# Optimization experiments

Hardware: AMD Instinct MI355X
Metric: run time of the kernel (lower is better)

Reference implementation:

```python
import jax, jax.numpy as jnp
import numpy as np

INPUT_DIM = 384
H1, H2, BOTTLENECK = 512, 216, 10
NUM_ANNOTATORS = 2316
BATCH = 16384


def setup_inputs() -> dict:
    key = jax.random.key(0)
    ks = jax.random.split(key, 9)

    def lin(k, fan_in, fan_out):
        # torch nn.Linear default init: U(-1/sqrt(fan_in), 1/sqrt(fan_in))
        bound = 1.0 / np.sqrt(fan_in)
        kw, kb = jax.random.split(k)
        W = jax.random.uniform(kw, (fan_in, fan_out), jnp.float32, -bound, bound)
        b = jax.random.uniform(kb, (fan_out,), jnp.float32, -bound, bound)
        return W, b

    x = jax.random.normal(ks[0], (BATCH, INPUT_DIM), jnp.float32)
    W1, b1 = lin(ks[1], INPUT_DIM, H1)
    W2, b2 = lin(ks[2], H1, H2)
    W3, b3 = lin(ks[3], H2, BOTTLENECK)
    # 2316 heads of Linear(10, 1) stacked into a single (10, 2316) matrix + (2316,) bias
    Wh, bh = lin(ks[4], BOTTLENECK, NUM_ANNOTATORS)
    return {"x": x, "W1": W1, "b1": b1, "W2": W2, "b2": b2,
            "W3": W3, "b3": b3, "Wh": Wh, "bh": bh}


def reference(x, W1, b1, W2, b2, W3, b3, Wh, bh):
    # shared encoder (dropout is identity in eval mode)
    h = jax.nn.relu(x @ W1 + b1)            # [B, 512]
    h = jax.nn.relu(h @ W2 + b2)            # [B, 216]
    f = jax.nn.relu(h @ W3 + b3)            # [B, 10]
    # 2316 per-annotator heads fused into one GEMM: [B,10] @ [10,2316] + [2316]
    return f @ Wh + bh                      # [B, 2316]
```

## Files before the change

kernel.cpp:

```cpp
#include <hip/hip_runtime.h>
#include <hip/hip_bf16.h>
#include <stdint.h>

using f32x4  = __attribute__((ext_vector_type(4))) float;
using bf16x8 = __attribute__((ext_vector_type(8))) __bf16;
using u16x4  = __attribute__((ext_vector_type(4))) unsigned short;
using u16x8  = __attribute__((ext_vector_type(8))) unsigned short;

#define DEVFN static __device__ __forceinline__

constexpr int IND = 384, N1 = 512, N2R = 216, N2 = 256, NB = 10, NA = 2316;
constexpr int BATCH = 16384;
constexpr int RB  = 64;
constexpr int NC1 = 12;
constexpr int NC2 = 16;
constexpr int K3  = 224;

constexpr int WS_W1  = 0;
constexpr int WS_W2  = WS_W1 + NC1 * N1 * 32;
constexpr int WS_W3  = WS_W2 + NC2 * N2 * 32;
constexpr size_t WS_F_BYTE = 708864;
constexpr size_t WS_NEED   = WS_F_BYTE + (size_t)BATCH * 12 * 4;

constexpr int XT_OFF = 0;      constexpr int XT_ST = 784;
constexpr int W1T    = 51200;
constexpr int H1_OFF = 0;      constexpr int H1_ST = 1040;
constexpr int W2T    = 66560;
constexpr int H2_OFF = 0;      constexpr int H2_ST = 528;
constexpr int W3_OFF = 115712;
constexpr int F_OFF  = 122880; constexpr int F_ST  = 48;
constexpr int B1L    = 149504;
constexpr int B2L    = 151552;
constexpr int B3L    = 152576;
constexpr int LDS_E  = 152640;

DEVFN unsigned short bf16u(float f) {
    __hip_bfloat16 h = __float2bfloat16(f);
    unsigned short u; __builtin_memcpy(&u, &h, 2); return u;
}

DEVFN void mfma16(f32x4& d, bf16x8 a, bf16x8 b) {
    d = __builtin_amdgcn_mfma_f32_16x16x32_bf16(a, b, d, 0, 0, 0);
}

DEVFN void gll16(const void* g, void* lds) {
    __builtin_amdgcn_global_load_lds((const __attribute__((address_space(1))) void*)g,
                                     (__attribute__((address_space(3))) void*)lds, 16, 0, 0);
}

DEVFN void wait_vm4()   { asm volatile("s_waitcnt vmcnt(4)" ::: "memory"); }
DEVFN void wait_vm2()   { asm volatile("s_waitcnt vmcnt(2)" ::: "memory"); }
DEVFN void wait_vm0()   { asm volatile("s_waitcnt vmcnt(0)" ::: "memory"); }
DEVFN void wait_lgkm0() { asm volatile("s_waitcnt lgkmcnt(0)" ::: "memory"); }

__global__ __launch_bounds__(256)
void cvt_weights(const float* __restrict__ W1, const float* __restrict__ W2,
                 const float* __restrict__ W3,
                 unsigned short* __restrict__ ws)
{
    const int bid = blockIdx.x, tid = threadIdx.x;
    if (bid < 48) {
        const int c = bid >> 2, o = bid & 3;
        #pragma unroll
        for (int half = 0; half < 2; ++half) {
            const int col = half * 256 + tid;
            u16x8 v;
            #pragma unroll
            for (int s7 = 0; s7 < 8; ++s7)
                v[s7] = bf16u(W1[(size_t)(c * 32 + o * 8 + s7) * N1 + col]);
            *(u16x8*)(ws + WS_W1 + c * 16384 + col * 32 + ((o ^ (col & 3)) << 3)) = v;
        }
    } else if (bid < 112) {
        const int t = bid - 48;
        const int c = t >> 2, o = t & 3;
        const int col = tid;
        u16x8 v;
        #pragma unroll
        for (int s7 = 0; s7 < 8; ++s7) {
            int k = c * 32 + o * 8 + s7;
            v[s7] = (col < N2R) ? bf16u(W2[(size_t)k * N2R + col]) : (unsigned short)0;
        }
        *(u16x8*)(ws + WS_W2 + c * 8192 + col * 32 + ((o ^ (col & 3)) << 3)) = v;
    } else {
        for (int i = tid; i < 16 * K3; i += 256) {
            int col = i / K3, s = i - col * K3;
            int sb = s >> 5, r = s & 31;
            int k = sb * 32 + (((r >> 3) ^ (col & 3)) << 3) + (r & 7);
            float v = (col < NB && k < 216) ? W3[k * NB + col] : 0.f;
            ws[WS_W3 + i] = bf16u(v);
        }
    }
}

__global__ __launch_bounds__(512)
void encoder(const float* __restrict__ x,
             const float* __restrict__ b1g, const float* __restrict__ b2g,
             const float* __restrict__ b3g,
             const unsigned short* __restrict__ ws,
             float* __restrict__ fout)
{
    __shared__ __attribute__((aligned(16))) unsigned char smem[LDS_E];
    const int tid  = threadIdx.x;
    const int wave = tid >> 6;
    const int lane = tid & 63;
    const int l16  = lane & 15;
    const int lk   = lane >> 4;
    const int wr   = wave >> 2;
    const int wc   = wave & 3;
    const int row0 = blockIdx.x * RB;

    {
        const float4* xg = (const float4*)(x + (size_t)row0 * IND);
        #pragma unroll
        for (int i = 0; i < 12; ++i) {
            int j = tid + i * 512;
            float4 v = xg[j];
            int el = j * 4, r = el / IND, c = el - r * IND;
            u16x4 h;
            h[0] = bf16u(v.x); h[1] = bf16u(v.y); h[2] = bf16u(v.z); h[3] = bf16u(v.w);
            *(u16x4*)(smem + XT_OFF + r * XT_ST + c * 2) = h;
        }
        *(float*)(smem + B1L + tid * 4) = b1g[tid];
        if (tid < 256) *(float*)(smem + B2L + tid * 4) = (tid < N2R) ? b2g[tid] : 0.f;
        if (tid < 16)  *(float*)(smem + B3L + tid * 4) = (tid < NB)  ? b3g[tid] : 0.f;
    }
    __syncthreads();

    const unsigned char* wsW1 = (const unsigned char*)(ws + WS_W1);
    f32x4 acc1[2][8] = {};

    #pragma unroll
    for (int cc = 0; cc < 2; ++cc)
        #pragma unroll
        for (int o = 0; o < 4; ++o) {
            int wb = o * 8192 + wave * 1024;
            gll16(wsW1 + cc * 32768 + wb + lane * 16, smem + W1T + cc * 32768 + wb);
        }
    for (int c = 0; c < NC1; ++c) {
        if (c + 1 < NC1) wait_vm4(); else wait_vm0();
        __builtin_amdgcn_s_barrier();
        if (c + 2 < NC1) {
            const unsigned char* src = wsW1 + (size_t)(c + 2) * 32768;
            const int nxt = W1T + ((c + 2) % 3) * 32768;
            #pragma unroll
            for (int o = 0; o < 4; ++o) {
                int wb = o * 8192 + wave * 1024;
                gll16(src + wb + lane * 16, smem + nxt + wb);
            }
        }
        const int cur = W1T + (c % 3) * 32768;
        const int k0 = c * 32;
        bf16x8 a0 = *(const bf16x8*)(smem + XT_OFF + (wr * 32 + l16)      * XT_ST + (k0 + lk * 8) * 2);
        bf16x8 a1 = *(const bf16x8*)(smem + XT_OFF + (wr * 32 + 16 + l16) * XT_ST + (k0 + lk * 8) * 2);
        #pragma unroll
        for (int n = 0; n < 8; ++n) {
            int col = wc * 128 + n * 16 + l16;
            bf16x8 b = *(const bf16x8*)(smem + cur + col * 64 + ((lk ^ (col & 3)) << 4));
            mfma16(acc1[0][n], a0, b);
            mfma16(acc1[1][n], a1, b);
        }
    }
    __builtin_amdgcn_s_barrier();
    #pragma unroll
    for (int m = 0; m < 2; ++m)
        #pragma unroll
        for (int n = 0; n < 8; ++n) {
            int col = wc * 128 + n * 16 + l16;
            float bias = *(const float*)(smem + B1L + col * 4);
            #pragma unroll
            for (int e = 0; e < 4; ++e) {
                float v = fmaxf(acc1[m][n][e] + bias, 0.f);
                *(unsigned short*)(smem + H1_OFF + (wr * 32 + m * 16 + lk * 4 + e) * H1_ST + col * 2) = bf16u(v);
            }
        }
    wait_lgkm0();
    __builtin_amdgcn_s_barrier();

    const unsigned char* wsW2 = (const unsigned char*)(ws + WS_W2);
    f32x4 acc2[2][4] = {};

    #pragma unroll
    for (int cc = 0; cc < 2; ++cc)
        #pragma unroll
        for (int o = 0; o < 2; ++o) {
            int wb = o * 8192 + wave * 1024;
            gll16(wsW2 + cc * 16384 + wb + lane * 16, smem + W2T + cc * 16384 + wb);
        }
    for (int c = 0; c < NC2; ++c) {
        if (c + 1 < NC2) wait_vm2(); else wait_vm0();
        __builtin_amdgcn_s_barrier();
        if (c + 2 < NC2) {
            const unsigned char* src = wsW2 + (size_t)(c + 2) * 16384;
            const int nxt = W2T + ((c + 2) % 3) * 16384;
            #pragma unroll
            for (int o = 0; o < 2; ++o) {
                int wb = o * 8192 + wave * 1024;
                gll16(src + wb + lane * 16, smem + nxt + wb);
            }
        }
        const int cur = W2T + (c % 3) * 16384;
        const int k0 = c * 32;
        bf16x8 a0 = *(const bf16x8*)(smem + H1_OFF + (wr * 32 + l16)      * H1_ST + (k0 + lk * 8) * 2);
        bf16x8 a1 = *(const bf16x8*)(smem + H1_OFF + (wr * 32 + 16 + l16) * H1_ST + (k0 + lk * 8) * 2);
        #pragma unroll
        for (int n = 0; n < 4; ++n) {
            int col = wc * 64 + n * 16 + l16;
            bf16x8 b = *(const bf16x8*)(smem + cur + col * 64 + ((lk ^ (col & 3)) << 4));
            mfma16(acc2[0][n], a0, b);
            mfma16(acc2[1][n], a1, b);
        }
    }
    __builtin_amdgcn_s_barrier();
    #pragma unroll
    for (int m = 0; m < 2; ++m)
        #pragma unroll
        for (int n = 0; n < 4; ++n) {
            int col = wc * 64 + n * 16 + l16;
            float bias = *(const float*)(smem + B2L + col * 4);
            #pragma unroll
            for (int e = 0; e < 4; ++e) {
                float v = fmaxf(acc2[m][n][e] + bias, 0.f);
                *(unsigned short*)(smem + H2_OFF + (wr * 32 + m * 16 + lk * 4 + e) * H2_ST + col * 2) = bf16u(v);
            }
        }
    if (wave < 7)
        gll16((const unsigned char*)(ws + WS_W3) + wave * 1024 + lane * 16, smem + W3_OFF + wave * 1024);
    __syncthreads();

    f32x4 acc3[2] = {};
    #pragma unroll
    for (int c = 0; c < 7; ++c) {
        const int k0 = c * 32;
        bf16x8 a0 = *(const bf16x8*)(smem + H2_OFF + (wr * 32 + l16)      * H2_ST + (k0 + lk * 8) * 2);
        bf16x8 a1 = *(const bf16x8*)(smem + H2_OFF + (wr * 32 + 16 + l16) * H2_ST + (k0 + lk * 8) * 2);
        bf16x8 b  = *(const bf16x8*)(smem + W3_OFF + l16 * 448 + c * 64 + ((lk ^ (l16 & 3)) << 4));
        mfma16(acc3[0], a0, b);
        mfma16(acc3[1], a1, b);
    }
    if (wc == 0 && l16 < NB) {
        float bias = *(const float*)(smem + B3L + l16 * 4);
        #pragma unroll
        for (int m = 0; m < 2; ++m)
            #pragma unroll
            for (int e = 0; e < 4; ++e) {
                float v = fmaxf(acc3[m][e] + bias, 0.f);
                *(float*)(smem + F_OFF + (wr * 32 + m * 16 + lk * 4 + e) * F_ST + l16 * 4) = v;
            }
    }
    if (wc == 1 && l16 < 2) {
        #pragma unroll
        for (int m = 0; m < 2; ++m)
            #pragma unroll
            for (int e = 0; e < 4; ++e)
                *(float*)(smem + F_OFF + (wr * 32 + m * 16 + lk * 4 + e) * F_ST + (10 + l16) * 4) = 0.f;
    }
    __syncthreads();

    if (tid < 192)
        *(f32x4*)(fout + (size_t)row0 * 12 + tid * 4) = *(const f32x4*)(smem + F_OFF + tid * 16);
}

__global__ __launch_bounds__(512)
void head(const float* __restrict__ fin, const float* __restrict__ bhg,
          const float* __restrict__ WhG, float* __restrict__ out)
{
    const int tid = threadIdx.x;
    const int r0  = blockIdx.x * 32;
    const int j0  = tid;
    const int j1  = 512 + tid;
    const bool has1 = (j1 < 579);

    float w0[10][4];
    float4 bh0 = ((const float4*)bhg)[j0];
    #pragma unroll
    for (int k = 0; k < 10; ++k) {
        f32x4 q = *(const f32x4*)(WhG + (size_t)k * NA + j0 * 4);
        w0[k][0] = q[0]; w0[k][1] = q[1]; w0[k][2] = q[2]; w0[k][3] = q[3];
    }
    float w1[10][4];
    float4 bh1 = make_float4(0.f, 0.f, 0.f, 0.f);
    if (has1) {
        #pragma unroll
        for (int k = 0; k < 10; ++k) {
            f32x4 q = *(const f32x4*)(WhG + (size_t)k * NA + j1 * 4);
            w1[k][0] = q[0]; w1[k][1] = q[1]; w1[k][2] = q[2]; w1[k][3] = q[3];
        }
        bh1 = ((const float4*)bhg)[j1];
    }

    #pragma unroll 1
    for (int rg = 0; rg < 8; ++rg) {
        const float* __restrict__ fr = fin + (size_t)(r0 + rg * 4) * 12;
        float fv[4][10];
        #pragma unroll
        for (int rr = 0; rr < 4; ++rr)
            #pragma unroll
            for (int k = 0; k < 10; ++k)
                fv[rr][k] = fr[rr * 12 + k];

        float ac[4][4];
        #pragma unroll
        for (int rr = 0; rr < 4; ++rr) {
            ac[rr][0] = bh0.x; ac[rr][1] = bh0.y; ac[rr][2] = bh0.z; ac[rr][3] = bh0.w;
            #pragma unroll
            for (int k = 0; k < 10; ++k) {
                ac[rr][0] = fmaf(fv[rr][k], w0[k][0], ac[rr][0]);
                ac[rr][1] = fmaf(fv[rr][k], w0[k][1], ac[rr][1]);
                ac[rr][2] = fmaf(fv[rr][k], w0[k][2], ac[rr][2]);
                ac[rr][3] = fmaf(fv[rr][k], w0[k][3], ac[rr][3]);
            }
        }
        #pragma unroll
        for (int rr = 0; rr < 4; ++rr) {
            float4 o;
            o.x = ac[rr][0]; o.y = ac[rr][1]; o.z = ac[rr][2]; o.w = ac[rr][3];
            *(float4*)(out + (size_t)(r0 + rg * 4 + rr) * NA + j0 * 4) = o;
        }
        if (has1) {
            float ac1[4][4];
            #pragma unroll
            for (int rr = 0; rr < 4; ++rr) {
                ac1[rr][0] = bh1.x; ac1[rr][1] = bh1.y; ac1[rr][2] = bh1.z; ac1[rr][3] = bh1.w;
                #pragma unroll
                for (int k = 0; k < 10; ++k) {
                    ac1[rr][0] = fmaf(fv[rr][k], w1[k][0], ac1[rr][0]);
                    ac1[rr][1] = fmaf(fv[rr][k], w1[k][1], ac1[rr][1]);
                    ac1[rr][2] = fmaf(fv[rr][k], w1[k][2], ac1[rr][2]);
                    ac1[rr][3] = fmaf(fv[rr][k], w1[k][3], ac1[rr][3]);
                }
            }
            #pragma unroll
            for (int rr = 0; rr < 4; ++rr) {
                float4 o;
                o.x = ac1[rr][0]; o.y = ac1[rr][1]; o.z = ac1[rr][2]; o.w = ac1[rr][3];
                *(float4*)(out + (size_t)(r0 + rg * 4 + rr) * NA + j1 * 4) = o;
            }
        }
    }
}

extern "C" void kernel_launch(void* const* d_in, const int* in_sizes, int n_in,
                              void* d_out, int out_size, void* d_ws, size_t ws_size,
                              hipStream_t stream)
{
    const float* x  = (const float*)d_in[0];
    const float* W1 = (const float*)d_in[1];
    const float* b1 = (const float*)d_in[2];
    const float* W2 = (const float*)d_in[3];
    const float* b2 = (const float*)d_in[4];
    const float* W3 = (const float*)d_in[5];
    const float* b3 = (const float*)d_in[6];
    const float* Wh = (const float*)d_in[7];
    const float* bh = (const float*)d_in[8];
    unsigned short* ws = (unsigned short*)d_ws;
    float* fbuf = (float*)((char*)d_ws + WS_F_BYTE);
    float* out = (float*)d_out;

    if (ws_size < WS_NEED) return;

    cvt_weights<<<dim3(113), dim3(256), 0, stream>>>(W1, W2, W3, ws);
    encoder<<<dim3(BATCH / RB), dim3(512), 0, stream>>>(x, b1, b2, b3, ws, fbuf);
    head<<<dim3(512), dim3(512), 0, stream>>>(fbuf, bh, Wh, out);
}
```

Measured before the change: 54.57 us.

## Fuse annotator head GEMM into encoder kernel, reading features from LDS

Merges the head kernel into the encoder so each 64-row block computes its bottleneck features in LDS and then immediately produces the 2316-column output for those rows. This removes the intermediate feature buffer round-trip through global memory and one kernel launch. In exchange the head weights are reloaded per block (256 blocks instead of 512) and the output-store phase now runs serialized after the encoder in the same block, which has high LDS use and so low occupancy to hide store latency.

Result: faster. 53.09 us (-2.7%).

```diff
diff --git a/kernel.cpp b/kernel.cpp
--- a/kernel.cpp
+++ b/kernel.cpp
@@ -19,8 +19,7 @@
 constexpr int WS_W1  = 0;
 constexpr int WS_W2  = WS_W1 + NC1 * N1 * 32;
 constexpr int WS_W3  = WS_W2 + NC2 * N2 * 32;
-constexpr size_t WS_F_BYTE = 708864;
-constexpr size_t WS_NEED   = WS_F_BYTE + (size_t)BATCH * 12 * 4;
+constexpr size_t WS_NEED = 708864;
 
 constexpr int XT_OFF = 0;      constexpr int XT_ST = 784;
 constexpr int W1T    = 51200;
@@ -93,11 +92,12 @@
 }
 
 __global__ __launch_bounds__(512)
-void encoder(const float* __restrict__ x,
-             const float* __restrict__ b1g, const float* __restrict__ b2g,
-             const float* __restrict__ b3g,
-             const unsigned short* __restrict__ ws,
-             float* __restrict__ fout)
+void fused_mlp(const float* __restrict__ x,
+               const float* __restrict__ b1g, const float* __restrict__ b2g,
+               const float* __restrict__ b3g,
+               const unsigned short* __restrict__ ws,
+               const float* __restrict__ WhG, const float* __restrict__ bhg,
+               float* __restrict__ out)
 {
     __shared__ __attribute__((aligned(16))) unsigned char smem[LDS_E];
     const int tid  = threadIdx.x;
@@ -247,38 +247,20 @@
                 *(float*)(smem + F_OFF + (wr * 32 + m * 16 + lk * 4 + e) * F_ST + l16 * 4) = v;
             }
     }
-    if (wc == 1 && l16 < 2) {
-        #pragma unroll
-        for (int m = 0; m < 2; ++m)
-            #pragma unroll
-            for (int e = 0; e < 4; ++e)
-                *(float*)(smem + F_OFF + (wr * 32 + m * 16 + lk * 4 + e) * F_ST + (10 + l16) * 4) = 0.f;
-    }
     __syncthreads();
 
-    if (tid < 192)
-        *(f32x4*)(fout + (size_t)row0 * 12 + tid * 4) = *(const f32x4*)(smem + F_OFF + tid * 16);
-}
-
-__global__ __launch_bounds__(512)
-void head(const float* __restrict__ fin, const float* __restrict__ bhg,
-          const float* __restrict__ WhG, float* __restrict__ out)
-{
-    const int tid = threadIdx.x;
-    const int r0  = blockIdx.x * 32;
-    const int j0  = tid;
-    const int j1  = 512 + tid;
+    const int j0 = tid;
+    const int j1 = 512 + tid;
     const bool has1 = (j1 < 579);
 
-    float w0[10][4];
+    float w0[10][4], w1[10][4];
     float4 bh0 = ((const float4*)bhg)[j0];
+    float4 bh1 = make_float4(0.f, 0.f, 0.f, 0.f);
     #pragma unroll
     for (int k = 0; k < 10; ++k) {
         f32x4 q = *(const f32x4*)(WhG + (size_t)k * NA + j0 * 4);
         w0[k][0] = q[0]; w0[k][1] = q[1]; w0[k][2] = q[2]; w0[k][3] = q[3];
     }
-    float w1[10][4];
-    float4 bh1 = make_float4(0.f, 0.f, 0.f, 0.f);
     if (has1) {
         #pragma unroll
         for (int k = 0; k < 10; ++k) {
@@ -289,15 +271,18 @@
     }
 
     #pragma unroll 1
-    for (int rg = 0; rg < 8; ++rg) {
-        const float* __restrict__ fr = fin + (size_t)(r0 + rg * 4) * 12;
+    for (int rg = 0; rg < 16; ++rg) {
         float fv[4][10];
         #pragma unroll
-        for (int rr = 0; rr < 4; ++rr)
-            #pragma unroll
-            for (int k = 0; k < 10; ++k)
-                fv[rr][k] = fr[rr * 12 + k];
-
+        for (int rr = 0; rr < 4; ++rr) {
+            const unsigned char* fb = smem + F_OFF + (rg * 4 + rr) * F_ST;
+            f32x4 p0 = *(const f32x4*)(fb);
+            f32x4 p1 = *(const f32x4*)(fb + 16);
+            float2 p2 = *(const float2*)(fb + 32);
+            fv[rr][0] = p0[0]; fv[rr][1] = p0[1]; fv[rr][2] = p0[2]; fv[rr][3] = p0[3];
+            fv[rr][4] = p1[0]; fv[rr][5] = p1[1]; fv[rr][6] = p1[2]; fv[rr][7] = p1[3];
+            fv[rr][8] = p2.x;  fv[rr][9] = p2.y;
+        }
         float ac[4][4];
         #pragma unroll
         for (int rr = 0; rr < 4; ++rr) {
@@ -314,7 +299,7 @@
         for (int rr = 0; rr < 4; ++rr) {
             float4 o;
             o.x = ac[rr][0]; o.y = ac[rr][1]; o.z = ac[rr][2]; o.w = ac[rr][3];
-            *(float4*)(out + (size_t)(r0 + rg * 4 + rr) * NA + j0 * 4) = o;
+            *(float4*)(out + (size_t)(row0 + rg * 4 + rr) * NA + j0 * 4) = o;
         }
         if (has1) {
             float ac1[4][4];
@@ -333,7 +318,7 @@
             for (int rr = 0; rr < 4; ++rr) {
                 float4 o;
                 o.x = ac1[rr][0]; o.y = ac1[rr][1]; o.z = ac1[rr][2]; o.w = ac1[rr][3];
-                *(float4*)(out + (size_t)(r0 + rg * 4 + rr) * NA + j1 * 4) = o;
+                *(float4*)(out + (size_t)(row0 + rg * 4 + rr) * NA + j1 * 4) = o;
             }
         }
     }
@@ -353,12 +338,10 @@
     const float* Wh = (const float*)d_in[7];
     const float* bh = (const float*)d_in[8];
     unsigned short* ws = (unsigned short*)d_ws;
-    float* fbuf = (float*)((char*)d_ws + WS_F_BYTE);
     float* out = (float*)d_out;
 
     if (ws_size < WS_NEED) return;
 
     cvt_weights<<<dim3(113), dim3(256), 0, stream>>>(W1, W2, W3, ws);
-    encoder<<<dim3(BATCH / RB), dim3(512), 0, stream>>>(x, b1, b2, b3, ws, fbuf);
-    head<<<dim3(512), dim3(512), 0, stream>>>(fbuf, bh, Wh, out);
-}
+    fused_mlp<<<dim3(BATCH / RB), dim3(512), 0, stream>>>(x, b1, b2, b3, ws, Wh, bh, out);
+}
```
